# Optimization experiments

Hardware: AMD Instinct MI355X
Metric: run time of the kernel (lower is better)

## Reference

```python
import jax, jax.numpy as jnp
import numpy as np

N_NODES = 100000
N_EDGES = 500000
DIM = 128
HID = 128

def setup_inputs() -> dict:
    key = jax.random.key(0)
    k1, k2, k3, k4, k5, k6 = jax.random.split(key, 6)
    z = jax.random.normal(k1, (N_NODES, DIM), dtype=jnp.float32)
    edge_index = jax.random.randint(k2, (2, N_EDGES), 0, N_NODES, dtype=jnp.int64)
    # Linear params (torch default init: U(-1/sqrt(fan_in), 1/sqrt(fan_in)))
    b1_lim = 1.0 / np.sqrt(3 * DIM)
    b2_lim = 1.0 / np.sqrt(HID)
    W1 = jax.random.uniform(k3, (3 * DIM, HID), jnp.float32, -b1_lim, b1_lim)
    b1 = jax.random.uniform(k4, (HID,), jnp.float32, -b1_lim, b1_lim)
    W2 = jax.random.uniform(k5, (HID, 1), jnp.float32, -b2_lim, b2_lim)
    b2 = jax.random.uniform(k6, (1,), jnp.float32, -b2_lim, b2_lim)
    return {"z": z, "edge_index": edge_index, "W1": W1, "b1": b1, "W2": W2, "b2": b2}

def reference(z, edge_index, W1, b1, W2, b2):
    u, v = edge_index[0], edge_index[1]
    zu = z[u]                      # [E, dim]
    zv = z[v]                      # [E, dim]
    feat = jnp.concatenate([zu, zv, jnp.abs(zu - zv)], axis=1)  # [E, 3*dim]
    h = jax.nn.relu(feat @ W1 + b1)   # [E, hid]
    logit = h @ W2 + b2               # [E, 1]
    return logit.squeeze(-1)          # [E]
```

## Files before the change

kernel.cpp:

```cpp
#include <hip/hip_runtime.h>
#include <hip/hip_bf16.h>
#include <cstdint>


typedef __bf16 bf16_t;
typedef __bf16 bf16x8 __attribute__((ext_vector_type(8)));
typedef float  floatx4 __attribute__((ext_vector_type(4)));

#define DIM 128
#define K3 384
#define E_TILE 64
#define N_KSTEP 12
#define N_NTILE 8

__global__ void cast_z_kernel(const float* __restrict__ z, bf16_t* __restrict__ zb, int n) {
    int idx = (blockIdx.x * 256 + threadIdx.x) * 8;
    if (idx + 8 > n) return;
    const float4* src = reinterpret_cast<const float4*>(z + idx);
    float4 a = src[0], b = src[1];
    bf16x8 o;
    o[0] = (bf16_t)a.x; o[1] = (bf16_t)a.y; o[2] = (bf16_t)a.z; o[3] = (bf16_t)a.w;
    o[4] = (bf16_t)b.x; o[5] = (bf16_t)b.y; o[6] = (bf16_t)b.z; o[7] = (bf16_t)b.w;
    *reinterpret_cast<bf16x8*>(zb + idx) = o;
}

__global__ void pack_w1_kernel(const float* __restrict__ W1, bf16_t* __restrict__ Wp) {
    int f = blockIdx.x * 256 + threadIdx.x;
    if (f >= N_KSTEP * N_NTILE * 64) return;
    int lane = f & 63;
    int nt   = (f >> 6) & 7;
    int ks   = f >> 9;
    int n  = nt * 16 + (lane & 15);
    int k0 = ks * 32 + (lane >> 4) * 8;
    bf16x8 o;
#pragma unroll
    for (int j = 0; j < 8; ++j) o[j] = (bf16_t)W1[(k0 + j) * DIM + n];
    reinterpret_cast<bf16x8*>(Wp)[f] = o;
}

template <bool PRECAST>
__global__ __launch_bounds__(256, 3)
void decode_kernel(const void* __restrict__ zsrc,
                   const int* __restrict__ ei,
                   const bf16_t* __restrict__ Wp,
                   const float* __restrict__ b1,
                   const float* __restrict__ W2,
                   const float* __restrict__ b2,
                   float* __restrict__ out, int E) {
    __shared__ float red[2][E_TILE];

    const int tid  = threadIdx.x;
    const int wave = tid >> 6, lane = tid & 63;
    const int wm = wave >> 1, wn = wave & 1;
    const int l15 = lane & 15, quad = lane >> 4;
    const int ebase = blockIdx.x * E_TILE;

    int nu[2], nv[2];
#pragma unroll
    for (int mt = 0; mt < 2; ++mt) {
        int e = ebase + wm * 32 + mt * 16 + l15;
        if (e >= E) e = E - 1;
        nu[mt] = ei[e];
        nv[mt] = ei[E + e];
    }

    bf16x8 uz[2][4], vz[2][4];
    if (PRECAST) {
        const bf16_t* zb = (const bf16_t*)zsrc;
#pragma unroll
        for (int mt = 0; mt < 2; ++mt) {
#pragma unroll
            for (int c = 0; c < 4; ++c) {
                uz[mt][c] = *reinterpret_cast<const bf16x8*>(
                    zb + (size_t)nu[mt] * DIM + c * 32 + quad * 8);
                vz[mt][c] = *reinterpret_cast<const bf16x8*>(
                    zb + (size_t)nv[mt] * DIM + c * 32 + quad * 8);
            }
        }
    } else {
        const float* zf = (const float*)zsrc;
#pragma unroll
        for (int mt = 0; mt < 2; ++mt) {
#pragma unroll
            for (int c = 0; c < 4; ++c) {
                const float4* pu = reinterpret_cast<const float4*>(
                    zf + (size_t)nu[mt] * DIM + c * 32 + quad * 8);
                const float4* pv = reinterpret_cast<const float4*>(
                    zf + (size_t)nv[mt] * DIM + c * 32 + quad * 8);
                float4 a = pu[0], b = pu[1];
                bf16x8 o;
                o[0] = (bf16_t)a.x; o[1] = (bf16_t)a.y; o[2] = (bf16_t)a.z; o[3] = (bf16_t)a.w;
                o[4] = (bf16_t)b.x; o[5] = (bf16_t)b.y; o[6] = (bf16_t)b.z; o[7] = (bf16_t)b.w;
                uz[mt][c] = o;
                a = pv[0]; b = pv[1];
                o[0] = (bf16_t)a.x; o[1] = (bf16_t)a.y; o[2] = (bf16_t)a.z; o[3] = (bf16_t)a.w;
                o[4] = (bf16_t)b.x; o[5] = (bf16_t)b.y; o[6] = (bf16_t)b.z; o[7] = (bf16_t)b.w;
                vz[mt][c] = o;
            }
        }
    }

    float b1v[4], w2v[4];
#pragma unroll
    for (int nt = 0; nt < 4; ++nt) {
        int n = (wn * 4 + nt) * 16 + l15;
        b1v[nt] = b1[n];
        w2v[nt] = W2[n];
    }

    const bf16x8* WpF = reinterpret_cast<const bf16x8*>(Wp);
    const int wbase = wn * 4;

    floatx4 acc[2][4];
#pragma unroll
    for (int mt = 0; mt < 2; ++mt)
#pragma unroll
        for (int nt = 0; nt < 4; ++nt) acc[mt][nt] = (floatx4)0.0f;

    auto loadB = [&](bf16x8* dst, int ks) {
#pragma unroll
        for (int nt = 0; nt < 4; ++nt)
            dst[nt] = WpF[(ks * N_NTILE + wbase + nt) * 64 + lane];
    };
    auto afragf = [&](int mt, int ks) -> bf16x8 {
        if (ks < 4) return uz[mt][ks];
        if (ks < 8) return vz[mt][ks - 4];
        bf16x8 u = uz[mt][ks - 8], v = vz[mt][ks - 8];
        bf16x8 d;
#pragma unroll
        for (int j = 0; j < 8; ++j)
            d[j] = (bf16_t)fabsf((float)u[j] - (float)v[j]);
        return d;
    };

    bf16x8 bcur[4], bnext[4];
    loadB(bcur, 0);
    loadB(bnext, 1);
#pragma unroll
    for (int ks = 0; ks < N_KSTEP; ++ks) {
        bf16x8 bpre[4];
        if (ks + 2 < N_KSTEP) loadB(bpre, ks + 2);
#pragma unroll
        for (int mt = 0; mt < 2; ++mt) {
            bf16x8 af = afragf(mt, ks);
#pragma unroll
            for (int nt = 0; nt < 4; ++nt)
                acc[mt][nt] = __builtin_amdgcn_mfma_f32_16x16x32_bf16(
                    af, bcur[nt], acc[mt][nt], 0, 0, 0);
        }
        if (ks + 1 < N_KSTEP) {
#pragma unroll
            for (int nt = 0; nt < 4; ++nt) bcur[nt] = bnext[nt];
        }
        if (ks + 2 < N_KSTEP) {
#pragma unroll
            for (int nt = 0; nt < 4; ++nt) bnext[nt] = bpre[nt];
        }
    }

    float partial[2][4];
#pragma unroll
    for (int mt = 0; mt < 2; ++mt)
#pragma unroll
        for (int r = 0; r < 4; ++r) {
            float s = 0.f;
#pragma unroll
            for (int nt = 0; nt < 4; ++nt) {
                float h = acc[mt][nt][r] + b1v[nt];
                h = fmaxf(h, 0.f);
                s += h * w2v[nt];
            }
            s += __shfl_xor(s, 1);
            s += __shfl_xor(s, 2);
            s += __shfl_xor(s, 4);
            s += __shfl_xor(s, 8);
            partial[mt][r] = s;
        }
    if (l15 == 0) {
#pragma unroll
        for (int mt = 0; mt < 2; ++mt)
#pragma unroll
            for (int r = 0; r < 4; ++r) {
                int m = wm * 32 + mt * 16 + quad * 4 + r;
                red[wn][m] = partial[mt][r];
            }
    }
    __syncthreads();

    if (tid < E_TILE) {
        int e = ebase + tid;
        if (e < E) out[e] = red[0][tid] + red[1][tid] + b2[0];
    }
}

extern "C" void kernel_launch(void* const* d_in, const int* in_sizes, int n_in,
                              void* d_out, int out_size, void* d_ws, size_t ws_size,
                              hipStream_t stream) {
    const float* z  = (const float*)d_in[0];
    const int*   ei = (const int*)d_in[1];
    const float* W1 = (const float*)d_in[2];
    const float* b1 = (const float*)d_in[3];
    const float* W2 = (const float*)d_in[4];
    const float* b2 = (const float*)d_in[5];
    float* out = (float*)d_out;

    const int E  = in_sizes[1] / 2;
    const int zn = in_sizes[0];

    const size_t zb_bytes = (size_t)zn * sizeof(bf16_t);
    const size_t wp_bytes = (size_t)N_KSTEP * N_NTILE * 64 * 16;
    const bool precast = ws_size >= zb_bytes + wp_bytes;

    bf16_t* zb = (bf16_t*)d_ws;
    bf16_t* wp = precast ? (bf16_t*)((char*)d_ws + zb_bytes) : (bf16_t*)d_ws;

    hipLaunchKernelGGL(pack_w1_kernel, dim3((N_KSTEP * N_NTILE * 64 + 255) / 256),
                       dim3(256), 0, stream, W1, wp);

    const int nblocks = (E + E_TILE - 1) / E_TILE;
    if (precast) {
        hipLaunchKernelGGL(cast_z_kernel, dim3((zn / 8 + 255) / 256), dim3(256),
                           0, stream, z, zb, zn);
        hipLaunchKernelGGL((decode_kernel<true>), dim3(nblocks), dim3(256), 0,
                           stream, (const void*)zb, ei, wp, b1, W2, b2, out, E);
    } else {
        hipLaunchKernelGGL((decode_kernel<false>), dim3(nblocks), dim3(256), 0,
                           stream, (const void*)z, ei, wp, b1, W2, b2, out, E);
    }
}
```

Before: 213.3 us.

## Persistent decode kernel with LDS-staged W1 and prefetched next-tile gathers

Turns the decode kernel into a persistent kernel: a fixed grid of 256 blocks of 512 threads loops over 256-edge tiles. Each block stages the packed W1 fragments (about 96KB) into shared memory once, so B operands come from LDS instead of global memory. Each wave now covers all 128 hidden columns, which removes the cross-wave shared-memory reduction and lets each wave write its outputs directly. Each wave also prefetches the next tile's edge indices and gathers its z rows while the current tile's MFMAs run, hiding gather latency. The cost is a large LDS footprint and high register pressure (16 accumulators plus the u/v fragments), and with only 256 blocks on the machine occupancy and latency hiding may be limited.

```diff
diff --git a/kernel.cpp b/kernel.cpp
--- a/kernel.cpp
+++ b/kernel.cpp
@@ -8,10 +8,10 @@
 typedef float  floatx4 __attribute__((ext_vector_type(4)));
 
 #define DIM 128
-#define K3 384
-#define E_TILE 64
+#define E_TILE 256
 #define N_KSTEP 12
 #define N_NTILE 8
+#define GRID_B 256
 
 __global__ void cast_z_kernel(const float* __restrict__ z, bf16_t* __restrict__ zb, int n) {
     int idx = (blockIdx.x * 256 + threadIdx.x) * 8;
@@ -39,7 +39,7 @@
 }
 
 template <bool PRECAST>
-__global__ __launch_bounds__(256, 3)
+__global__ __launch_bounds__(512, 2)
 void decode_kernel(const void* __restrict__ zsrc,
                    const int* __restrict__ ei,
                    const bf16_t* __restrict__ Wp,
@@ -47,149 +47,154 @@
                    const float* __restrict__ W2,
                    const float* __restrict__ b2,
                    float* __restrict__ out, int E) {
-    __shared__ float red[2][E_TILE];
-
-    const int tid  = threadIdx.x;
+    __shared__ __align__(16) bf16_t Bsm[N_KSTEP * N_NTILE * 64 * 8];
+
+    const int tid = threadIdx.x;
+
+    {
+        const uint4* src = reinterpret_cast<const uint4*>(Wp);
+        uint4* dst = reinterpret_cast<uint4*>(Bsm);
+#pragma unroll
+        for (int i = 0; i < 12; ++i)
+            dst[i * 512 + tid] = src[i * 512 + tid];
+    }
+    __syncthreads();
+
     const int wave = tid >> 6, lane = tid & 63;
-    const int wm = wave >> 1, wn = wave & 1;
     const int l15 = lane & 15, quad = lane >> 4;
-    const int ebase = blockIdx.x * E_TILE;
-
-    int nu[2], nv[2];
-#pragma unroll
-    for (int mt = 0; mt < 2; ++mt) {
-        int e = ebase + wm * 32 + mt * 16 + l15;
-        if (e >= E) e = E - 1;
-        nu[mt] = ei[e];
-        nv[mt] = ei[E + e];
-    }
-
-    bf16x8 uz[2][4], vz[2][4];
-    if (PRECAST) {
-        const bf16_t* zb = (const bf16_t*)zsrc;
-#pragma unroll
-        for (int mt = 0; mt < 2; ++mt) {
-#pragma unroll
-            for (int c = 0; c < 4; ++c) {
-                uz[mt][c] = *reinterpret_cast<const bf16x8*>(
-                    zb + (size_t)nu[mt] * DIM + c * 32 + quad * 8);
-                vz[mt][c] = *reinterpret_cast<const bf16x8*>(
-                    zb + (size_t)nv[mt] * DIM + c * 32 + quad * 8);
-            }
-        }
-    } else {
-        const float* zf = (const float*)zsrc;
-#pragma unroll
-        for (int mt = 0; mt < 2; ++mt) {
-#pragma unroll
-            for (int c = 0; c < 4; ++c) {
-                const float4* pu = reinterpret_cast<const float4*>(
-                    zf + (size_t)nu[mt] * DIM + c * 32 + quad * 8);
-                const float4* pv = reinterpret_cast<const float4*>(
-                    zf + (size_t)nv[mt] * DIM + c * 32 + quad * 8);
-                float4 a = pu[0], b = pu[1];
-                bf16x8 o;
-                o[0] = (bf16_t)a.x; o[1] = (bf16_t)a.y; o[2] = (bf16_t)a.z; o[3] = (bf16_t)a.w;
-                o[4] = (bf16_t)b.x; o[5] = (bf16_t)b.y; o[6] = (bf16_t)b.z; o[7] = (bf16_t)b.w;
-                uz[mt][c] = o;
-                a = pv[0]; b = pv[1];
-                o[0] = (bf16_t)a.x; o[1] = (bf16_t)a.y; o[2] = (bf16_t)a.z; o[3] = (bf16_t)a.w;
-                o[4] = (bf16_t)b.x; o[5] = (bf16_t)b.y; o[6] = (bf16_t)b.z; o[7] = (bf16_t)b.w;
-                vz[mt][c] = o;
-            }
-        }
-    }
-
-    float b1v[4], w2v[4];
-#pragma unroll
-    for (int nt = 0; nt < 4; ++nt) {
-        int n = (wn * 4 + nt) * 16 + l15;
+
+    float b1v[8], w2v[8];
+#pragma unroll
+    for (int nt = 0; nt < 8; ++nt) {
+        int n = nt * 16 + l15;
         b1v[nt] = b1[n];
         w2v[nt] = W2[n];
     }
-
-    const bf16x8* WpF = reinterpret_cast<const bf16x8*>(Wp);
-    const int wbase = wn * 4;
-
-    floatx4 acc[2][4];
-#pragma unroll
-    for (int mt = 0; mt < 2; ++mt)
-#pragma unroll
-        for (int nt = 0; nt < 4; ++nt) acc[mt][nt] = (floatx4)0.0f;
+    const float bias2 = b2[0];
+
+    const int ntiles = (E + E_TILE - 1) / E_TILE;
+
+    auto gatherChunk = [&](bf16x8& du, bf16x8& dv, int nu, int nv, int c) {
+        if (PRECAST) {
+            const bf16_t* zb = (const bf16_t*)zsrc;
+            du = *reinterpret_cast<const bf16x8*>(zb + (size_t)nu * DIM + c * 32 + quad * 8);
+            dv = *reinterpret_cast<const bf16x8*>(zb + (size_t)nv * DIM + c * 32 + quad * 8);
+        } else {
+            const float* zf = (const float*)zsrc;
+            const float4* pu = reinterpret_cast<const float4*>(zf + (size_t)nu * DIM + c * 32 + quad * 8);
+            const float4* pv = reinterpret_cast<const float4*>(zf + (size_t)nv * DIM + c * 32 + quad * 8);
+            float4 a = pu[0], b = pu[1];
+            bf16x8 o;
+            o[0] = (bf16_t)a.x; o[1] = (bf16_t)a.y; o[2] = (bf16_t)a.z; o[3] = (bf16_t)a.w;
+            o[4] = (bf16_t)b.x; o[5] = (bf16_t)b.y; o[6] = (bf16_t)b.z; o[7] = (bf16_t)b.w;
+            du = o;
+            a = pv[0]; b = pv[1];
+            o[0] = (bf16_t)a.x; o[1] = (bf16_t)a.y; o[2] = (bf16_t)a.z; o[3] = (bf16_t)a.w;
+            o[4] = (bf16_t)b.x; o[5] = (bf16_t)b.y; o[6] = (bf16_t)b.z; o[7] = (bf16_t)b.w;
+            dv = o;
+        }
+    };
+
+    auto loadIdx = [&](int t, int mt, int& nu, int& nv) {
+        int e = t * E_TILE + wave * 32 + mt * 16 + l15;
+        if (e >= E) e = E - 1;
+        nu = ei[e];
+        nv = ei[E + e];
+    };
 
     auto loadB = [&](bf16x8* dst, int ks) {
 #pragma unroll
-        for (int nt = 0; nt < 4; ++nt)
-            dst[nt] = WpF[(ks * N_NTILE + wbase + nt) * 64 + lane];
+        for (int nt = 0; nt < 8; ++nt)
+            dst[nt] = *reinterpret_cast<const bf16x8*>(
+                &Bsm[(size_t)((ks * N_NTILE + nt) * 64 + lane) * 8]);
     };
-    auto afragf = [&](int mt, int ks) -> bf16x8 {
-        if (ks < 4) return uz[mt][ks];
-        if (ks < 8) return vz[mt][ks - 4];
-        bf16x8 u = uz[mt][ks - 8], v = vz[mt][ks - 8];
-        bf16x8 d;
-#pragma unroll
-        for (int j = 0; j < 8; ++j)
-            d[j] = (bf16_t)fabsf((float)u[j] - (float)v[j]);
-        return d;
-    };
-
-    bf16x8 bcur[4], bnext[4];
-    loadB(bcur, 0);
-    loadB(bnext, 1);
-#pragma unroll
-    for (int ks = 0; ks < N_KSTEP; ++ks) {
-        bf16x8 bpre[4];
-        if (ks + 2 < N_KSTEP) loadB(bpre, ks + 2);
-#pragma unroll
-        for (int mt = 0; mt < 2; ++mt) {
-            bf16x8 af = afragf(mt, ks);
-#pragma unroll
-            for (int nt = 0; nt < 4; ++nt)
-                acc[mt][nt] = __builtin_amdgcn_mfma_f32_16x16x32_bf16(
-                    af, bcur[nt], acc[mt][nt], 0, 0, 0);
+
+    bf16x8 uz[2][4], vz[2][4];
+    {
+        int nu[2], nv[2];
+#pragma unroll
+        for (int mt = 0; mt < 2; ++mt) loadIdx(blockIdx.x, mt, nu[mt], nv[mt]);
+#pragma unroll
+        for (int mt = 0; mt < 2; ++mt)
+#pragma unroll
+            for (int c = 0; c < 4; ++c)
+                gatherChunk(uz[mt][c], vz[mt][c], nu[mt], nv[mt], c);
+    }
+
+    for (int t = blockIdx.x; t < ntiles; t += GRID_B) {
+        int nnu[2], nnv[2];
+#pragma unroll
+        for (int mt = 0; mt < 2; ++mt) loadIdx(t + GRID_B, mt, nnu[mt], nnv[mt]);
+
+        floatx4 acc[2][8];
+#pragma unroll
+        for (int mt = 0; mt < 2; ++mt)
+#pragma unroll
+            for (int nt = 0; nt < 8; ++nt) acc[mt][nt] = (floatx4)0.0f;
+
+#pragma unroll
+        for (int c = 0; c < 4; ++c) {
+            {
+                bf16x8 bc[8];
+                loadB(bc, c);
+#pragma unroll
+                for (int mt = 0; mt < 2; ++mt)
+#pragma unroll
+                    for (int nt = 0; nt < 8; ++nt)
+                        acc[mt][nt] = __builtin_amdgcn_mfma_f32_16x16x32_bf16(
+                            uz[mt][c], bc[nt], acc[mt][nt], 0, 0, 0);
+            }
+            {
+                bf16x8 bc[8];
+                loadB(bc, 4 + c);
+#pragma unroll
+                for (int mt = 0; mt < 2; ++mt)
+#pragma unroll
+                    for (int nt = 0; nt < 8; ++nt)
+                        acc[mt][nt] = __builtin_amdgcn_mfma_f32_16x16x32_bf16(
+                            vz[mt][c], bc[nt], acc[mt][nt], 0, 0, 0);
+            }
+            {
+                bf16x8 bc[8];
+                loadB(bc, 8 + c);
+#pragma unroll
+                for (int mt = 0; mt < 2; ++mt) {
+                    bf16x8 u = uz[mt][c], v = vz[mt][c];
+                    bf16x8 d;
+#pragma unroll
+                    for (int j = 0; j < 8; ++j)
+                        d[j] = (bf16_t)fabsf((float)u[j] - (float)v[j]);
+#pragma unroll
+                    for (int nt = 0; nt < 8; ++nt)
+                        acc[mt][nt] = __builtin_amdgcn_mfma_f32_16x16x32_bf16(
+                            d, bc[nt], acc[mt][nt], 0, 0, 0);
+                }
+            }
+#pragma unroll
+            for (int mt = 0; mt < 2; ++mt)
+                gatherChunk(uz[mt][c], vz[mt][c], nnu[mt], nnv[mt], c);
         }
-        if (ks + 1 < N_KSTEP) {
-#pragma unroll
-            for (int nt = 0; nt < 4; ++nt) bcur[nt] = bnext[nt];
-        }
-        if (ks + 2 < N_KSTEP) {
-#pragma unroll
-            for (int nt = 0; nt < 4; ++nt) bnext[nt] = bpre[nt];
-        }
-    }
-
-    float partial[2][4];
-#pragma unroll
-    for (int mt = 0; mt < 2; ++mt)
-#pragma unroll
-        for (int r = 0; r < 4; ++r) {
-            float s = 0.f;
-#pragma unroll
-            for (int nt = 0; nt < 4; ++nt) {
-                float h = acc[mt][nt][r] + b1v[nt];
-                h = fmaxf(h, 0.f);
-                s += h * w2v[nt];
-            }
-            s += __shfl_xor(s, 1);
-            s += __shfl_xor(s, 2);
-            s += __shfl_xor(s, 4);
-            s += __shfl_xor(s, 8);
-            partial[mt][r] = s;
-        }
-    if (l15 == 0) {
+
 #pragma unroll
         for (int mt = 0; mt < 2; ++mt)
 #pragma unroll
             for (int r = 0; r < 4; ++r) {
-                int m = wm * 32 + mt * 16 + quad * 4 + r;
-                red[wn][m] = partial[mt][r];
-            }
-    }
-    __syncthreads();
-
-    if (tid < E_TILE) {
-        int e = ebase + tid;
-        if (e < E) out[e] = red[0][tid] + red[1][tid] + b2[0];
+                float s = 0.f;
+#pragma unroll
+                for (int nt = 0; nt < 8; ++nt) {
+                    float h = acc[mt][nt][r] + b1v[nt];
+                    h = fmaxf(h, 0.f);
+                    s += h * w2v[nt];
+                }
+                s += __shfl_xor(s, 1);
+                s += __shfl_xor(s, 2);
+                s += __shfl_xor(s, 4);
+                s += __shfl_xor(s, 8);
+                if (l15 == 0) {
+                    int e = t * E_TILE + wave * 32 + mt * 16 + quad * 4 + r;
+                    if (e < E) out[e] = s + bias2;
+                }
+            }
     }
 }
 
@@ -217,14 +222,13 @@
     hipLaunchKernelGGL(pack_w1_kernel, dim3((N_KSTEP * N_NTILE * 64 + 255) / 256),
                        dim3(256), 0, stream, W1, wp);
 
-    const int nblocks = (E + E_TILE - 1) / E_TILE;
     if (precast) {
         hipLaunchKernelGGL(cast_z_kernel, dim3((zn / 8 + 255) / 256), dim3(256),
                            0, stream, z, zb, zn);
-        hipLaunchKernelGGL((decode_kernel<true>), dim3(nblocks), dim3(256), 0,
+        hipLaunchKernelGGL((decode_kernel<true>), dim3(GRID_B), dim3(512), 0,
                            stream, (const void*)zb, ei, wp, b1, W2, b2, out, E);
     } else {
-        hipLaunchKernelGGL((decode_kernel<false>), dim3(nblocks), dim3(256), 0,
+        hipLaunchKernelGGL((decode_kernel<false>), dim3(GRID_B), dim3(512), 0,
                            stream, (const void*)z, ei, wp, b1, W2, b2, out, E);
     }
 }
```

New measurement: 397.3 us. 1.86x slower.
